# Kernel tuning notes

Hardware: AMD Instinct MI355X
Metric: run time of the kernel (lower is better)

## Reference

```python
import jax, jax.numpy as jnp
import numpy as np

B, T, D = 4, 1024, 1024
NEXP, TOPK = 8, 2
N = B * T
# eval capacity: floor(TOPK * 2.0 * N / NEXP) = 2048, already even and >= min_capacity
CAP = 2048
LN_EPS = 1e-5


def setup_inputs() -> dict:
    key = jax.random.key(0)
    ks = jax.random.split(key, 4)
    x = jax.random.normal(ks[0], (B, T, D), jnp.float32)
    w_g = jax.random.normal(ks[1], (D, NEXP), jnp.float32) * 0.02
    c_fc = jax.random.normal(ks[2], (NEXP, D, 4 * D), jnp.float32) * 0.02
    c_proj = jax.random.normal(ks[3], (NEXP, 4 * D, D), jnp.float32) * 0.02
    ln_w = jnp.ones((D,), jnp.float32)
    ln_b = jnp.zeros((D,), jnp.float32)
    return {"x": x, "w_g": w_g, "c_fc": c_fc, "c_proj": c_proj, "ln_w": ln_w, "ln_b": ln_b}


def moe_forward(x, w_g, c_fc, c_proj, ln_w, ln_b):
    xf = x.reshape(N, D)
    # --- Router ---
    logits = xf @ w_g                                   # [N, E]
    topk_vals, topk_idx = jax.lax.top_k(logits, TOPK)   # [N, K]
    masked = jnp.full_like(logits, -jnp.inf)
    masked = masked.at[jnp.arange(N)[:, None], topk_idx].set(topk_vals)
    probs = jax.nn.softmax(masked, axis=-1)             # [N, E]

    # capacity-based ranking (slot 0 for all tokens first, then slot 1, ...)
    onehot = jax.nn.one_hot(topk_idx, NEXP, dtype=jnp.int32)     # [N, K, E]
    exp_mask = jnp.transpose(onehot, (1, 0, 2))                  # [K, N, E]
    rank = jnp.cumsum(exp_mask.reshape(TOPK * N, NEXP), axis=0) - 1
    rank = rank.reshape(TOPK, N, NEXP)
    exp_mask = exp_mask * (rank < CAP).astype(jnp.int32)         # drop overflow
    rank_tok = jnp.sum(exp_mask * rank, axis=-1)                 # [K, N]
    exp_w = exp_mask.astype(probs.dtype) * probs[None]           # [K, N, E]
    rank_oh = jax.nn.one_hot(rank_tok, CAP, dtype=probs.dtype)   # [K, N, C]
    cb_weight = jnp.einsum('kne,knc->nec', exp_w, rank_oh)       # [N, E, C]
    sec_mask = (cb_weight != 0).astype(x.dtype)                  # dispatch mask

    # --- dispatch -> experts -> combine ---
    xb = jnp.einsum('nec,nd->ecd', sec_mask, xf)                 # [E, C, D]
    h = jax.nn.gelu(jnp.einsum('ecd,edf->ecf', xb, c_fc), approximate=False)
    eo = jnp.einsum('ecf,efd->ecd', h, c_proj)                   # [E, C, D]
    out = jnp.einsum('nec,ecd->nd', cb_weight, eo)               # [N, D]

    # --- LayerNorm ---
    mu = out.mean(-1, keepdims=True)
    var = out.var(-1, keepdims=True)
    out = (out - mu) / jnp.sqrt(var + LN_EPS) * ln_w + ln_b
    return out.reshape(B, T, D)


def reference(x, w_g, c_fc, c_proj, ln_w, ln_b):
    return moe_forward(x, w_g, c_fc, c_proj, ln_w, ln_b)
```

## Files before the change

### kernel.cpp

```cpp
#include <hip/hip_runtime.h>
#include <math.h>

#define NEXP 8
#define CAP 2048
#define NTOK 4096
#define DDIM 1024
#define FDIM 4096

typedef __bf16 bf16x8 __attribute__((ext_vector_type(8)));
typedef float f32x4 __attribute__((ext_vector_type(4)));
typedef unsigned short u16x8 __attribute__((ext_vector_type(8)));

__device__ __forceinline__ unsigned short f2bf(float f) {
    unsigned int u = __float_as_uint(f);
    u += 0x7FFFu + ((u >> 16) & 1u);
    return (unsigned short)(u >> 16);
}

__device__ __forceinline__ void gld_lds16(const void* g, void* l) {
    __builtin_amdgcn_global_load_lds((const __attribute__((address_space(1))) void*)g,
                                     (__attribute__((address_space(3))) void*)l, 16, 0, 0);
}

__global__ __launch_bounds__(256) void transpose_cvt64(const float* __restrict__ in,
                                                       unsigned short* __restrict__ out,
                                                       int R, int C) {
    __shared__ float tile[64][65];
    int e = blockIdx.z;
    const float* ip = in + (size_t)e * R * C;
    unsigned short* op = out + (size_t)e * R * C;
    int c0 = blockIdx.x * 64, r0 = blockIdx.y * 64;
    int t = threadIdx.x;
#pragma unroll
    for (int i = 0; i < 4; i++) {
        int rr = i * 16 + (t >> 4);
        int cc = (t & 15) * 4;
        float4 v = *(const float4*)&ip[(size_t)(r0 + rr) * C + c0 + cc];
        tile[rr][cc] = v.x; tile[rr][cc + 1] = v.y; tile[rr][cc + 2] = v.z; tile[rr][cc + 3] = v.w;
    }
    __syncthreads();
    int c = t >> 2, rb = (t & 3) * 16;
    u16x8 o0, o1;
#pragma unroll
    for (int j = 0; j < 8; j++) o0[j] = f2bf(tile[rb + j][c]);
#pragma unroll
    for (int j = 0; j < 8; j++) o1[j] = f2bf(tile[rb + 8 + j][c]);
    unsigned short* dst = op + (size_t)(c0 + c) * R + r0 + rb;
    *(u16x8*)dst = o0;
    *(u16x8*)(dst + 8) = o1;
}

__global__ __launch_bounds__(256) void router_kernel(const float* __restrict__ x,
                                                     const float* __restrict__ wg,
                                                     int2* __restrict__ e01,
                                                     float2* __restrict__ p01) {
    int wid = threadIdx.x >> 6, lane = threadIdx.x & 63;
    int n = blockIdx.x * 4 + wid;
    float acc[8];
#pragma unroll
    for (int i = 0; i < 8; i++) acc[i] = 0.f;
    const float4* xr = (const float4*)(x + (size_t)n * DDIM);
#pragma unroll
    for (int j = 0; j < 4; j++) {
        float4 xv = xr[j * 64 + lane];
        int base = (j * 64 + lane) * 4;
        float xs[4] = {xv.x, xv.y, xv.z, xv.w};
#pragma unroll
        for (int t = 0; t < 4; t++) {
            const float4* wr = (const float4*)(wg + (size_t)(base + t) * 8);
            float4 w0 = wr[0], w1 = wr[1];
            acc[0] += xs[t] * w0.x; acc[1] += xs[t] * w0.y;
            acc[2] += xs[t] * w0.z; acc[3] += xs[t] * w0.w;
            acc[4] += xs[t] * w1.x; acc[5] += xs[t] * w1.y;
            acc[6] += xs[t] * w1.z; acc[7] += xs[t] * w1.w;
        }
    }
#pragma unroll
    for (int off = 32; off > 0; off >>= 1) {
#pragma unroll
        for (int i = 0; i < 8; i++) acc[i] += __shfl_xor(acc[i], off);
    }
    if (lane == 0) {
        int i0 = 0; float v0 = acc[0];
#pragma unroll
        for (int q = 1; q < 8; q++) { if (acc[q] > v0) { v0 = acc[q]; i0 = q; } }
        int i1 = -1; float v1 = -3.0e38f;
#pragma unroll
        for (int q = 0; q < 8; q++) { if (q != i0 && acc[q] > v1) { v1 = acc[q]; i1 = q; } }
        float ea = expf(v0 - v0), eb = expf(v1 - v0);
        float inv = 1.f / (ea + eb);
        e01[n] = make_int2(i0, i1);
        p01[n] = make_float2(ea * inv, eb * inv);
    }
}

__global__ void assign_kernel(const int2* __restrict__ e01, int* __restrict__ counts,
                              int* __restrict__ assign_row, int* __restrict__ tok_slot) {
    int lane = threadIdx.x;
    int base[8];
#pragma unroll
    for (int i = 0; i < 8; i++) base[i] = 0;
    unsigned long long below = ((unsigned long long)1 << lane) - 1ull;
    int2 cur = e01[lane];
    for (int pass = 0; pass < 2; ++pass) {
        for (int t = 0; t < NTOK; t += 64) {
            int n = t + lane;
            int2 nxt;
            if (t + 64 < NTOK) nxt = e01[t + 64 + lane];
            else nxt = (pass == 0) ? e01[lane] : make_int2(0, 0);
            int ex = (pass == 0) ? cur.x : cur.y;
            int slot = -1;
#pragma unroll
            for (int q = 0; q < 8; q++) {
                unsigned long long m = __ballot(ex == q);
                if (ex == q) slot = base[q] + __popcll(m & below);
                base[q] += __popcll(m);
            }
            if (slot < CAP) {
                assign_row[ex * CAP + slot] = n;
                tok_slot[2 * n + pass] = slot;
            } else {
                tok_slot[2 * n + pass] = -1;
            }
            cur = nxt;
        }
    }
    if (lane < 8) counts[lane] = base[lane] > CAP ? CAP : base[lane];
}

__global__ __launch_bounds__(256) void gather_rows(const float* __restrict__ x,
                                                   const int* __restrict__ assign_row,
                                                   const int* __restrict__ counts,
                                                   unsigned short* __restrict__ xg) {
    int e = blockIdx.y;
    int wid = threadIdx.x >> 6, lane = threadIdx.x & 63;
    int slot = blockIdx.x * 4 + wid;
    if (slot >= counts[e]) return;
    int n = assign_row[e * CAP + slot];
    const float4* src = (const float4*)(x + (size_t)n * DDIM);
    unsigned short* dst = xg + ((size_t)e * CAP + slot) * DDIM;
#pragma unroll
    for (int j = 0; j < 4; j++) {
        float4 v = src[j * 64 + lane];
        ushort4 o;
        o.x = f2bf(v.x); o.y = f2bf(v.y); o.z = f2bf(v.z); o.w = f2bf(v.w);
        *(ushort4*)(dst + (size_t)(j * 64 + lane) * 4) = o;
    }
}

template <int WM, int WN, bool GELU>
__global__ __launch_bounds__(WM * WN * 64, 4) void gemm_db(const unsigned short* __restrict__ A,
                                                           const unsigned short* __restrict__ Bt,
                                                           void* __restrict__ Cout,
                                                           const int* __restrict__ counts,
                                                           int Mcap, int Ncols, int K) {
    constexpr int T = WM * WN * 64;
    constexpr int BM = WM * 64;
    constexpr int BN = WN * 64;
    constexpr int ABYTES = BM * 64;
    constexpr int BBYTES = BN * 64;
    constexpr int BUFB = ABYTES + BBYTES;
    constexpr int GA = (BM * 4) / T;
    constexpr int GB = (BN * 4) / T;
    __shared__ __align__(16) char smem[2 * BUFB];

    int gx = gridDim.x, gy = gridDim.y;
    int nwg = gx * gy * gridDim.z;
    int flat = blockIdx.x + gx * (blockIdx.y + gy * blockIdx.z);
    int cpx = nwg >> 3;
    int swz = (flat & 7) * cpx + (flat >> 3);
    int gxy = gx * gy;
    int e  = swz / gxy;
    int r2 = swz - e * gxy;
    int by = r2 / gx;
    int bx = r2 - by * gx;

    int cnt = counts[e];
    int row0 = by * BM;
    if (row0 >= cnt) return;
    int col0 = bx * BN;

    int tid = threadIdx.x;
    int w = tid >> 6, lane = tid & 63;
    int wm = w / WN, wn = w % WN;

    const unsigned short* Ab = A + ((size_t)e * Mcap + row0) * K;
    const unsigned short* Bb = Bt + ((size_t)e * Ncols + col0) * K;
    int NT = K >> 5;

    int kel = (((tid & 3) ^ ((tid >> 3) & 3)) * 8);
    int rA = tid >> 2;
    int ldst = tid * 16;

    int a_off[4], b_off[4];
    int c = lane >> 4;
#pragma unroll
    for (int m = 0; m < 4; m++) {
        int row = wm * 64 + m * 16 + (lane & 15);
        a_off[m] = row * 64 + ((c ^ ((row >> 1) & 3)) * 16);
    }
#pragma unroll
    for (int n = 0; n < 4; n++) {
        int row = wn * 64 + n * 16 + (lane & 15);
        b_off[n] = row * 64 + ((c ^ ((row >> 1) & 3)) * 16);
    }

    auto stage = [&](int tt) {
        int bb = (tt & 1) * BUFB;
        size_t kt = (size_t)tt * 32 + kel;
#pragma unroll
        for (int i = 0; i < GA; i++)
            gld_lds16(Ab + (size_t)(i * (T / 4) + rA) * K + kt, smem + bb + i * T * 16 + ldst);
#pragma unroll
        for (int i = 0; i < GB; i++)
            gld_lds16(Bb + (size_t)(i * (T / 4) + rA) * K + kt, smem + bb + ABYTES + i * T * 16 + ldst);
    };

    f32x4 acc[4][4] = {};

    stage(0);
    __builtin_amdgcn_sched_barrier(0);
    __syncthreads();

    for (int t = 0; t < NT; ++t) {
        const int bb = (t & 1) * BUFB;
        if (t + 1 < NT) stage(t + 1);
        __builtin_amdgcn_sched_barrier(0);
        bf16x8 af[4], bfr[4];
#pragma unroll
        for (int m = 0; m < 4; m++) af[m] = *(const bf16x8*)(smem + bb + a_off[m]);
#pragma unroll
        for (int n = 0; n < 4; n++) bfr[n] = *(const bf16x8*)(smem + bb + ABYTES + b_off[n]);
        __builtin_amdgcn_s_setprio(1);
#pragma unroll
        for (int m = 0; m < 4; m++)
#pragma unroll
            for (int n = 0; n < 4; n++)
                acc[m][n] = __builtin_amdgcn_mfma_f32_16x16x32_bf16(af[m], bfr[n], acc[m][n], 0, 0, 0);
        __builtin_amdgcn_s_setprio(0);
        __syncthreads();
    }

    unsigned short* Cb_h = (unsigned short*)Cout + ((size_t)e * Mcap + row0) * Ncols + col0;
    float* Cb_f = (float*)Cout + ((size_t)e * Mcap + row0) * Ncols + col0;
#pragma unroll
    for (int m = 0; m < 4; m++)
#pragma unroll
        for (int n = 0; n < 4; n++)
#pragma unroll
            for (int j = 0; j < 4; j++) {
                int lr = wm * 64 + m * 16 + ((lane >> 4) << 2) + j;
                int lc = wn * 64 + n * 16 + (lane & 15);
                float v = acc[m][n][j];
                if constexpr (GELU) {
                    float g = 0.5f * v * (1.0f + erff(v * 0.70710678118654752f));
                    Cb_h[(size_t)lr * Ncols + lc] = f2bf(g);
                } else {
                    Cb_f[(size_t)lr * Ncols + lc] = v;
                }
            }
}

__global__ __launch_bounds__(256) void combine_ln_kernel(const float* __restrict__ eo,
                                                         const int2* __restrict__ e01,
                                                         const float2* __restrict__ p01,
                                                         const int* __restrict__ tok_slot,
                                                         const float* __restrict__ lnw,
                                                         const float* __restrict__ lnb,
                                                         float* __restrict__ out) {
    int n = blockIdx.x, t = threadIdx.x;
    int2 e = e01[n];
    float2 p = p01[n];
    int s0 = tok_slot[2 * n], s1 = tok_slot[2 * n + 1];
    float o0 = 0.f, o1 = 0.f, o2 = 0.f, o3 = 0.f;
    if (s0 >= 0) {
        const float4* r = (const float4*)(eo + ((size_t)e.x * CAP + s0) * DDIM);
        float4 v = r[t];
        o0 += p.x * v.x; o1 += p.x * v.y; o2 += p.x * v.z; o3 += p.x * v.w;
    }
    if (s1 >= 0) {
        const float4* r = (const float4*)(eo + ((size_t)e.y * CAP + s1) * DDIM);
        float4 v = r[t];
        o0 += p.y * v.x; o1 += p.y * v.y; o2 += p.y * v.z; o3 += p.y * v.w;
    }
    float s = o0 + o1 + o2 + o3;
    float sq = o0 * o0 + o1 * o1 + o2 * o2 + o3 * o3;
#pragma unroll
    for (int off = 32; off > 0; off >>= 1) {
        s += __shfl_xor(s, off);
        sq += __shfl_xor(sq, off);
    }
    __shared__ float red[8];
    int wid = t >> 6, lane = t & 63;
    if (lane == 0) { red[wid] = s; red[4 + wid] = sq; }
    __syncthreads();
    s = red[0] + red[1] + red[2] + red[3];
    sq = red[4] + red[5] + red[6] + red[7];
    float mu = s * (1.f / DDIM);
    float var = sq * (1.f / DDIM) - mu * mu;
    float inv = rsqrtf(var + 1e-5f);
    const float4 w = ((const float4*)lnw)[t];
    const float4 b = ((const float4*)lnb)[t];
    float4 r;
    r.x = (o0 - mu) * inv * w.x + b.x;
    r.y = (o1 - mu) * inv * w.y + b.y;
    r.z = (o2 - mu) * inv * w.z + b.z;
    r.w = (o3 - mu) * inv * w.w + b.w;
    ((float4*)(out + (size_t)n * DDIM))[t] = r;
}

extern "C" void kernel_launch(void* const* d_in, const int* in_sizes, int n_in,
                              void* d_out, int out_size, void* d_ws, size_t ws_size,
                              hipStream_t stream) {
    const float* x   = (const float*)d_in[0];
    const float* wg  = (const float*)d_in[1];
    const float* cfc = (const float*)d_in[2];
    const float* cpr = (const float*)d_in[3];
    const float* lnw = (const float*)d_in[4];
    const float* lnb = (const float*)d_in[5];
    float* out = (float*)d_out;

    char* ws = (char*)d_ws;
    size_t off = 0;
    auto take = [&](size_t b) {
        char* p = ws + off;
        off += (b + 255) & ~(size_t)255;
        return p;
    };
    unsigned short* cfct = (unsigned short*)take((size_t)NEXP * FDIM * DDIM * 2);
    float* eo = (float*)cfct;
    unsigned short* cprt = (unsigned short*)take((size_t)NEXP * DDIM * FDIM * 2);
    unsigned short* xg   = (unsigned short*)take((size_t)NEXP * CAP * DDIM * 2);
    unsigned short* h    = (unsigned short*)take((size_t)NEXP * CAP * FDIM * 2);
    int2*   e01      = (int2*)take(NTOK * sizeof(int2));
    float2* p01      = (float2*)take(NTOK * sizeof(float2));
    int*    tok_slot = (int*)take((size_t)NTOK * 2 * 4);
    int*    assign_row = (int*)take((size_t)NEXP * CAP * 4);
    int*    counts   = (int*)take(256);

    transpose_cvt64<<<dim3(FDIM / 64, DDIM / 64, NEXP), 256, 0, stream>>>(cfc, cfct, DDIM, FDIM);
    transpose_cvt64<<<dim3(DDIM / 64, FDIM / 64, NEXP), 256, 0, stream>>>(cpr, cprt, FDIM, DDIM);
    router_kernel<<<NTOK / 4, 256, 0, stream>>>(x, wg, e01, p01);
    assign_kernel<<<1, 64, 0, stream>>>(e01, counts, assign_row, tok_slot);
    gather_rows<<<dim3(CAP / 4, NEXP), 256, 0, stream>>>(x, assign_row, counts, xg);
    gemm_db<2, 4, true ><<<dim3(FDIM / 256, CAP / 128, NEXP), 512, 0, stream>>>(xg, cfct, (void*)h, counts, CAP, FDIM, DDIM);
    gemm_db<2, 2, false><<<dim3(DDIM / 128, CAP / 128, NEXP), 256, 0, stream>>>(h, cprt, (void*)eo, counts, CAP, DDIM, FDIM);
    combine_ln_kernel<<<NTOK, 256, 0, stream>>>(eo, e01, p01, tok_slot, lnw, lnb, out);
}
```

Measured before the change: 357.5 us.

## Split-K the down-projection GEMM into bf16 partials summed in combine

The second expert GEMM (K=4096) is split into two K halves launched as separate workgroups, which doubles grid parallelism for the small-N projection. Each half writes a bf16 partial plane, and the combine/LayerNorm kernel sums the two planes while gathering. The first GEMM is changed from 128x256 tiles with 512 threads to 128x128 tiles with 256 threads. The trade is extra partial-output traffic and bf16 rounding of the partials, in exchange for better occupancy across the CUs.

After: 359.3 us. About the same (+0.5%).

```diff
diff --git a/kernel.cpp b/kernel.cpp
--- a/kernel.cpp
+++ b/kernel.cpp
@@ -15,6 +15,9 @@
     unsigned int u = __float_as_uint(f);
     u += 0x7FFFu + ((u >> 16) & 1u);
     return (unsigned short)(u >> 16);
+}
+__device__ __forceinline__ float bf2f(unsigned short h) {
+    return __uint_as_float(((unsigned int)h) << 16);
 }
 
 __device__ __forceinline__ void gld_lds16(const void* g, void* l) {
@@ -148,20 +151,14 @@
     }
 }
 
-template <int WM, int WN, bool GELU>
-__global__ __launch_bounds__(WM * WN * 64, 4) void gemm_db(const unsigned short* __restrict__ A,
-                                                           const unsigned short* __restrict__ Bt,
-                                                           void* __restrict__ Cout,
-                                                           const int* __restrict__ counts,
-                                                           int Mcap, int Ncols, int K) {
-    constexpr int T = WM * WN * 64;
-    constexpr int BM = WM * 64;
-    constexpr int BN = WN * 64;
-    constexpr int ABYTES = BM * 64;
-    constexpr int BBYTES = BN * 64;
-    constexpr int BUFB = ABYTES + BBYTES;
-    constexpr int GA = (BM * 4) / T;
-    constexpr int GB = (BN * 4) / T;
+template <bool GELU, int KC>
+__global__ __launch_bounds__(256, 4) void gemm_db(const unsigned short* __restrict__ A,
+                                                  const unsigned short* __restrict__ Bt,
+                                                  unsigned short* __restrict__ Cout,
+                                                  const int* __restrict__ counts,
+                                                  int Ncols, int Ktot) {
+    constexpr int ABYTES = 8192;
+    constexpr int BUFB = 16384;
     __shared__ __align__(16) char smem[2 * BUFB];
 
     int gx = gridDim.x, gy = gridDim.y;
@@ -170,23 +167,25 @@
     int cpx = nwg >> 3;
     int swz = (flat & 7) * cpx + (flat >> 3);
     int gxy = gx * gy;
-    int e  = swz / gxy;
-    int r2 = swz - e * gxy;
+    int zz = swz / gxy;
+    int r2 = swz - zz * gxy;
     int by = r2 / gx;
     int bx = r2 - by * gx;
+    int e = zz / KC, kc = zz % KC;
 
     int cnt = counts[e];
-    int row0 = by * BM;
+    int row0 = by * 128;
     if (row0 >= cnt) return;
-    int col0 = bx * BN;
+    int col0 = bx * 128;
+    const int Ksub = Ktot / KC;
+    const int NT = Ksub >> 5;
 
     int tid = threadIdx.x;
     int w = tid >> 6, lane = tid & 63;
-    int wm = w / WN, wn = w % WN;
-
-    const unsigned short* Ab = A + ((size_t)e * Mcap + row0) * K;
-    const unsigned short* Bb = Bt + ((size_t)e * Ncols + col0) * K;
-    int NT = K >> 5;
+    int wm = w >> 1, wn = w & 1;
+
+    const unsigned short* Ab = A + ((size_t)e * CAP + row0) * Ktot + (size_t)kc * Ksub;
+    const unsigned short* Bb = Bt + ((size_t)e * Ncols + col0) * Ktot + (size_t)kc * Ksub;
 
     int kel = (((tid & 3) ^ ((tid >> 3) & 3)) * 8);
     int rA = tid >> 2;
@@ -209,11 +208,11 @@
         int bb = (tt & 1) * BUFB;
         size_t kt = (size_t)tt * 32 + kel;
 #pragma unroll
-        for (int i = 0; i < GA; i++)
-            gld_lds16(Ab + (size_t)(i * (T / 4) + rA) * K + kt, smem + bb + i * T * 16 + ldst);
-#pragma unroll
-        for (int i = 0; i < GB; i++)
-            gld_lds16(Bb + (size_t)(i * (T / 4) + rA) * K + kt, smem + bb + ABYTES + i * T * 16 + ldst);
+        for (int i = 0; i < 2; i++)
+            gld_lds16(Ab + (size_t)(i * 64 + rA) * Ktot + kt, smem + bb + i * 4096 + ldst);
+#pragma unroll
+        for (int i = 0; i < 2; i++)
+            gld_lds16(Bb + (size_t)(i * 64 + rA) * Ktot + kt, smem + bb + ABYTES + i * 4096 + ldst);
     };
 
     f32x4 acc[4][4] = {};
@@ -241,8 +240,7 @@
         __syncthreads();
     }
 
-    unsigned short* Cb_h = (unsigned short*)Cout + ((size_t)e * Mcap + row0) * Ncols + col0;
-    float* Cb_f = (float*)Cout + ((size_t)e * Mcap + row0) * Ncols + col0;
+    unsigned short* Cb = Cout + (((size_t)(kc * NEXP + e) * CAP + row0)) * Ncols + col0;
 #pragma unroll
     for (int m = 0; m < 4; m++)
 #pragma unroll
@@ -254,34 +252,43 @@
                 float v = acc[m][n][j];
                 if constexpr (GELU) {
                     float g = 0.5f * v * (1.0f + erff(v * 0.70710678118654752f));
-                    Cb_h[(size_t)lr * Ncols + lc] = f2bf(g);
+                    Cb[(size_t)lr * Ncols + lc] = f2bf(g);
                 } else {
-                    Cb_f[(size_t)lr * Ncols + lc] = v;
+                    Cb[(size_t)lr * Ncols + lc] = f2bf(v);
                 }
             }
 }
 
-__global__ __launch_bounds__(256) void combine_ln_kernel(const float* __restrict__ eo,
+__global__ __launch_bounds__(256) void combine_ln_kernel(const unsigned short* __restrict__ pb,
                                                          const int2* __restrict__ e01,
                                                          const float2* __restrict__ p01,
                                                          const int* __restrict__ tok_slot,
                                                          const float* __restrict__ lnw,
                                                          const float* __restrict__ lnb,
                                                          float* __restrict__ out) {
+    const size_t PLANE = (size_t)NEXP * CAP * DDIM;
     int n = blockIdx.x, t = threadIdx.x;
     int2 e = e01[n];
     float2 p = p01[n];
     int s0 = tok_slot[2 * n], s1 = tok_slot[2 * n + 1];
     float o0 = 0.f, o1 = 0.f, o2 = 0.f, o3 = 0.f;
     if (s0 >= 0) {
-        const float4* r = (const float4*)(eo + ((size_t)e.x * CAP + s0) * DDIM);
-        float4 v = r[t];
-        o0 += p.x * v.x; o1 += p.x * v.y; o2 += p.x * v.z; o3 += p.x * v.w;
+        size_t base = ((size_t)e.x * CAP + s0) * DDIM;
+        ushort4 u0 = ((const ushort4*)(pb + base))[t];
+        ushort4 u1 = ((const ushort4*)(pb + PLANE + base))[t];
+        o0 += p.x * (bf2f(u0.x) + bf2f(u1.x));
+        o1 += p.x * (bf2f(u0.y) + bf2f(u1.y));
+        o2 += p.x * (bf2f(u0.z) + bf2f(u1.z));
+        o3 += p.x * (bf2f(u0.w) + bf2f(u1.w));
     }
     if (s1 >= 0) {
-        const float4* r = (const float4*)(eo + ((size_t)e.y * CAP + s1) * DDIM);
-        float4 v = r[t];
-        o0 += p.y * v.x; o1 += p.y * v.y; o2 += p.y * v.z; o3 += p.y * v.w;
+        size_t base = ((size_t)e.y * CAP + s1) * DDIM;
+        ushort4 u0 = ((const ushort4*)(pb + base))[t];
+        ushort4 u1 = ((const ushort4*)(pb + PLANE + base))[t];
+        o0 += p.y * (bf2f(u0.x) + bf2f(u1.x));
+        o1 += p.y * (bf2f(u0.y) + bf2f(u1.y));
+        o2 += p.y * (bf2f(u0.z) + bf2f(u1.z));
+        o3 += p.y * (bf2f(u0.w) + bf2f(u1.w));
     }
     float s = o0 + o1 + o2 + o3;
     float sq = o0 * o0 + o1 * o1 + o2 * o2 + o3 * o3;
@@ -328,7 +335,7 @@
         return p;
     };
     unsigned short* cfct = (unsigned short*)take((size_t)NEXP * FDIM * DDIM * 2);
-    float* eo = (float*)cfct;
+    unsigned short* pb = cfct;
     unsigned short* cprt = (unsigned short*)take((size_t)NEXP * DDIM * FDIM * 2);
     unsigned short* xg   = (unsigned short*)take((size_t)NEXP * CAP * DDIM * 2);
     unsigned short* h    = (unsigned short*)take((size_t)NEXP * CAP * FDIM * 2);
@@ -343,7 +350,7 @@
     router_kernel<<<NTOK / 4, 256, 0, stream>>>(x, wg, e01, p01);
     assign_kernel<<<1, 64, 0, stream>>>(e01, counts, assign_row, tok_slot);
     gather_rows<<<dim3(CAP / 4, NEXP), 256, 0, stream>>>(x, assign_row, counts, xg);
-    gemm_db<2, 4, true ><<<dim3(FDIM / 256, CAP / 128, NEXP), 512, 0, stream>>>(xg, cfct, (void*)h, counts, CAP, FDIM, DDIM);
-    gemm_db<2, 2, false><<<dim3(DDIM / 128, CAP / 128, NEXP), 256, 0, stream>>>(h, cprt, (void*)eo, counts, CAP, DDIM, FDIM);
-    combine_ln_kernel<<<NTOK, 256, 0, stream>>>(eo, e01, p01, tok_slot, lnw, lnb, out);
-}
+    gemm_db<true, 1><<<dim3(FDIM / 128, CAP / 128, NEXP), 256, 0, stream>>>(xg, cfct, h, counts, FDIM, DDIM);
+    gemm_db<false, 2><<<dim3(DDIM / 128, CAP / 128, NEXP * 2), 256, 0, stream>>>(h, cprt, pb, counts, DDIM, FDIM);
+    combine_ln_kernel<<<NTOK, 256, 0, stream>>>(pb, e01, p01, tok_slot, lnw, lnb, out);
+}
```
